# Kernel optimization log

Measured on AMD Instinct MI355X. Metric: run time of the kernel, lower is better.

## Reference

```python
import jax, jax.numpy as jnp
import numpy as np

N = 100_000
E = 1_600_000
IN, HID, HEADS, OUT = 128, 64, 4, 64
LAYER_DIMS = [(IN, HEADS, HID // HEADS), (HID, HEADS, HID // HEADS), (HID, 1, OUT)]
NEG_SLOPE = 0.2


def setup_inputs() -> dict:
    key = jax.random.key(0)
    ks = jax.random.split(key, 20)
    inp = {}
    inp["x"] = jax.random.normal(ks[0], (N, IN), dtype=jnp.float32)
    # edges with src != dst by construction (module removes self loops, then adds them)
    for i in range(3):
        src = jax.random.randint(ks[1 + 2 * i], (E,), 0, N, dtype=jnp.int32)
        off = jax.random.randint(ks[2 + 2 * i], (E,), 1, N, dtype=jnp.int32)
        dst = ((src + off) % N).astype(jnp.int32)
        inp[f"edge_index{i}"] = jnp.stack([src, dst])
    k = 7
    for i, (cin, h, c) in enumerate(LAYER_DIMS):
        ws = 1.0 / np.sqrt(cin)
        inp[f"Wl{i}"] = jax.random.normal(ks[k], (cin, h * c), dtype=jnp.float32) * ws; k += 1
        inp[f"bl{i}"] = jnp.zeros((h * c,), dtype=jnp.float32)
        inp[f"Wr{i}"] = jax.random.normal(ks[k], (cin, h * c), dtype=jnp.float32) * ws; k += 1
        inp[f"br{i}"] = jnp.zeros((h * c,), dtype=jnp.float32)
        inp[f"att{i}"] = jax.random.normal(ks[k], (h, c), dtype=jnp.float32) * (1.0 / np.sqrt(c)); k += 1
        inp[f"bias{i}"] = jnp.zeros((h * c,), dtype=jnp.float32)
    return inp


def _l1norm(x):
    return x / jnp.maximum(jnp.sum(jnp.abs(x), axis=1, keepdims=True), 1e-12)


def _gat2conv(x, ei, Wl, bl, Wr, br, att, bias, heads, out_c):
    n = x.shape[0]
    xl = (x @ Wl + bl).reshape(n, heads, out_c)  # source-side features (x_j)
    xr = (x @ Wr + br).reshape(n, heads, out_c)  # target-side features (x_i)
    src, dst = ei[0], ei[1]
    s = jax.nn.leaky_relu(xl[src] + xr[dst], NEG_SLOPE)      # [E', H, C]
    a = jnp.einsum('ehc,hc->eh', s, att)                      # [E', H]
    m = jax.ops.segment_max(a, dst, num_segments=n)           # segment softmax over edges per target
    e = jnp.exp(a - m[dst])
    den = jax.ops.segment_sum(e, dst, num_segments=n)
    alpha = e / (den[dst] + 1e-16)
    msg = (xl[src] * alpha[:, :, None]).reshape(-1, heads * out_c)
    return jax.ops.segment_sum(msg, dst, num_segments=n) + bias  # concat heads + bias


def _forward(x, eis, params):
    loop = jnp.arange(N, dtype=eis[0].dtype)
    self_loops = jnp.stack([loop, loop])
    num_layers = len(LAYER_DIMS)
    for i, ((cin, h, c), p) in enumerate(zip(LAYER_DIMS, params)):
        ei = jnp.concatenate([eis[i], self_loops], axis=1)  # add_self_loops
        new_x = _gat2conv(x, ei, *p, h, c)
        x = new_x
        if i != num_layers - 1:
            x = jax.nn.relu(new_x)
        x = _l1norm(x)  # F.normalize(x, p=1)
    x = x / jnp.maximum(jnp.linalg.norm(x, axis=1, keepdims=True), 1e-12)  # F.normalize (L2)
    return jax.nn.relu(x)


def reference(x, edge_index0, edge_index1, edge_index2,
              Wl0, bl0, Wr0, br0, att0, bias0,
              Wl1, bl1, Wr1, br1, att1, bias1,
              Wl2, bl2, Wr2, br2, att2, bias2):
    eis = (edge_index0, edge_index1, edge_index2)
    params = [(Wl0, bl0, Wr0, br0, att0, bias0),
              (Wl1, bl1, Wr1, br1, att1, bias1),
              (Wl2, bl2, Wr2, br2, att2, bias2)]
    return _forward(x, eis, params)
```

## Files before the change

### kernel.cpp

```cpp
#include <hip/hip_runtime.h>
#include <hip/hip_fp16.h>
#include <string.h>

#define NN 100000
#define EE 1600000
#define CAP 48
#define NBIN 196
#define BINSZ 512
#define BINCAP 10400
#define CHA 2048
#define NCA 782
#define GGX 391

typedef __fp16 h2v __attribute__((ext_vector_type(2)));
typedef __fp16 h4v __attribute__((ext_vector_type(4)));
typedef __fp16 half8 __attribute__((ext_vector_type(8)));
typedef float  f32x4 __attribute__((ext_vector_type(4)));

template<int CTRL>
__device__ __forceinline__ float dppadd(float x){
    int y = __builtin_amdgcn_update_dpp(0, __float_as_int(x), CTRL, 0xF, 0xF, true);
    return x + __int_as_float(y);
}
template<int H>
__device__ __forceinline__ float head_reduce16(float p){
    p = dppadd<0xB1>(p);
    p = dppadd<0x4E>(p);
    if constexpr (H == 1){
        p = dppadd<0x141>(p);
        p = dppadd<0x140>(p);
    }
    return p;
}
__device__ __forceinline__ float red16(float p){
    p = dppadd<0xB1>(p);
    p = dppadd<0x4E>(p);
    p = dppadd<0x141>(p);
    p = dppadd<0x140>(p);
    return p;
}


__global__ __launch_bounds__(256) void k_A(
    const int* __restrict__ e0, const int* __restrict__ e1, const int* __restrict__ e2,
    int* __restrict__ p0, int* __restrict__ p1, int* __restrict__ p2,
    int* __restrict__ tail)
{
    __shared__ int h4[4][NBIN];
    __shared__ int cur[NBIN];
    const int l = blockIdx.x / NCA, c = blockIdx.x % NCA;
    const int* ei = (l==0? e0 : l==1? e1 : e2);
    int* pr = (l==0? p0 : l==1? p1 : p2);
    const int base = c*CHA, n = min(CHA, EE-base);
    const int tid = threadIdx.x;
    const int wave = tid >> 6;
    for (int i=tid;i<4*NBIN;i+=256) ((int*)h4)[i]=0;
    __syncthreads();
    int dreg[CHA/256], sreg[CHA/256];
    #pragma unroll
    for (int j = 0; j < CHA/256; ++j){
        const int i = tid + j*256;
        if (i < n){ dreg[j] = ei[EE+base+i]; sreg[j] = ei[base+i]; }
        else { dreg[j] = -1; }
    }
    #pragma unroll
    for (int j = 0; j < CHA/256; ++j)
        if (dreg[j] >= 0) atomicAdd(&h4[wave][dreg[j]>>9],1);
    __syncthreads();
    if (tid < NBIN){
        const int t = h4[0][tid]+h4[1][tid]+h4[2][tid]+h4[3][tid];
        cur[tid] = t ? atomicAdd(&tail[l*NBIN+tid], t) : 0;
    }
    __syncthreads();
    #pragma unroll
    for (int j = 0; j < CHA/256; ++j){
        if (dreg[j] < 0) continue;
        const int d = dreg[j], s = sreg[j];
        const int bb = d>>9;
        const int r = atomicAdd(&cur[bb],1);
        if (r < BINCAP) pr[bb*BINCAP + r] = (s << 9) | (d & 511);
    }
}

__global__ __launch_bounds__(256) void k_B(
    const int* __restrict__ p0, const int* __restrict__ p1, const int* __restrict__ p2,
    const int* __restrict__ tail,
    int* __restrict__ c0, int* __restrict__ s0,
    int* __restrict__ c1, int* __restrict__ s1,
    int* __restrict__ c2, int* __restrict__ s2)
{
    __shared__ int cnt[BINSZ];
    __shared__ __align__(16) int sl[BINSZ*CAP];
    const int l = blockIdx.x / NBIN, b = blockIdx.x % NBIN;
    const int* pr = (l==0? p0 : l==1? p1 : p2) + (size_t)b*BINCAP;
    int* gc = (l==0? c0 : l==1? c1 : c2);
    int* gs = (l==0? s0 : l==1? s1 : s2);
    const int n0 = b*BINSZ;
    const int nn = min(BINSZ, NN - n0);
    const int tid = threadIdx.x;
    for (int i=tid;i<nn;i+=256){ cnt[i]=1; sl[i*CAP]= n0+i; }
    __syncthreads();
    const int ec = min(tail[l*NBIN+b], BINCAP);
    for (int i=tid;i<ec;i+=256){
        const int pv = pr[i];
        const int nd = pv & 511;
        const int p = atomicAdd(&cnt[nd],1);
        if (p < CAP) sl[nd*CAP+p] = pv >> 9;
    }
    __syncthreads();
    for (int i=tid;i<nn;i+=256) gc[n0+i] = cnt[i];
    const int t4 = nn*(CAP/4);
    int4* gs4 = (int4*)(gs + (size_t)n0*CAP);
    const int4* sl4 = (const int4*)sl;
    for (int i=tid;i<t4;i+=256) gs4[i] = sl4[i];
}


template<int CIN, typename TIN>
__global__ __launch_bounds__(256) void k_gemm(
    const TIN* __restrict__ x,
    const float* __restrict__ Wl, const float* __restrict__ bl,
    const float* __restrict__ Wr, const float* __restrict__ br,
    __half* __restrict__ xlh, float* __restrict__ xr)
{
    constexpr int KC = CIN / 32;
    const int tid = threadIdx.x;
    const int wave = tid >> 6, lane = tid & 63;
    const int m = lane & 15, g = lane >> 4;
    const int side = blockIdx.y;
    const float* __restrict__ W  = side ? Wr : Wl;
    const float* __restrict__ bb = side ? br : bl;

    half8 bf[4][KC];
    #pragma unroll
    for (int ct = 0; ct < 4; ++ct)
        #pragma unroll
        for (int kc = 0; kc < KC; ++kc)
            #pragma unroll
            for (int i = 0; i < 8; ++i)
                bf[ct][kc][i] = (__fp16)W[(kc*32 + g*8 + i)*64 + ct*16 + m];

    float bv[4];
    #pragma unroll
    for (int ct = 0; ct < 4; ++ct) bv[ct] = bb[ct*16 + m];

    const int stride = GGX * 64;
    for (int row0 = blockIdx.x*64 + wave*16; row0 < NN; row0 += stride){
        half8 a[KC];
        const TIN* xp = x + (size_t)(row0 + m) * CIN + g*8;
        #pragma unroll
        for (int kc = 0; kc < KC; ++kc){
            if constexpr (sizeof(TIN) == 4){
                const float4 u = *(const float4*)(xp + kc*32);
                const float4 v = *(const float4*)(xp + kc*32 + 4);
                a[kc][0]=(__fp16)u.x; a[kc][1]=(__fp16)u.y; a[kc][2]=(__fp16)u.z; a[kc][3]=(__fp16)u.w;
                a[kc][4]=(__fp16)v.x; a[kc][5]=(__fp16)v.y; a[kc][6]=(__fp16)v.z; a[kc][7]=(__fp16)v.w;
            } else {
                a[kc] = *(const half8*)(xp + kc*32);
            }
        }
        f32x4 acc0 = {0,0,0,0}, acc1 = {0,0,0,0}, acc2 = {0,0,0,0}, acc3 = {0,0,0,0};
        #pragma unroll
        for (int kc = 0; kc < KC; ++kc){
            acc0 = __builtin_amdgcn_mfma_f32_16x16x32_f16(a[kc], bf[0][kc], acc0, 0,0,0);
            acc1 = __builtin_amdgcn_mfma_f32_16x16x32_f16(a[kc], bf[1][kc], acc1, 0,0,0);
            acc2 = __builtin_amdgcn_mfma_f32_16x16x32_f16(a[kc], bf[2][kc], acc2, 0,0,0);
            acc3 = __builtin_amdgcn_mfma_f32_16x16x32_f16(a[kc], bf[3][kc], acc3, 0,0,0);
        }
        #pragma unroll
        for (int j = 0; j < 4; ++j){
            const size_t rb = (size_t)(row0 + 4*g + j)*64 + m;
            const float o0 = acc0[j] + bv[0];
            const float o1 = acc1[j] + bv[1];
            const float o2 = acc2[j] + bv[2];
            const float o3 = acc3[j] + bv[3];
            if (side){
                xr[rb]    = o0; xr[rb+16] = o1; xr[rb+32] = o2; xr[rb+48] = o3;
            } else {
                xlh[rb]    = __float2half_rn(o0);
                xlh[rb+16] = __float2half_rn(o1);
                xlh[rb+32] = __float2half_rn(o2);
                xlh[rb+48] = __float2half_rn(o3);
            }
        }
    }
}

template<int H, bool LAST>
__global__ __launch_bounds__(256) void k_fused(
    const int* __restrict__ cnt, const int* __restrict__ slots,
    const __half* __restrict__ xlh, const float* __restrict__ xr,
    const float* __restrict__ att, const float* __restrict__ bias,
    __half* __restrict__ o_h, float* __restrict__ o_f)
{
    const int lane = threadIdx.x & 63;
    const int sub = lane >> 4;
    const int c  = lane & 15;
    const int node = __builtin_amdgcn_readfirstlane(blockIdx.x * 4 + (threadIdx.x >> 6));
    if (node >= NN) return;
    constexpr float L2E = 1.44269504088896f;

    const float4 xr4 = *(const float4*)(xr + (size_t)node*64 + 4*c);
    const h2v xra = { (__fp16)xr4.x, (__fp16)xr4.y };
    const h2v xrb = { (__fp16)xr4.z, (__fp16)xr4.w };
    const float4 at4 = *(const float4*)(att + 4*c);
    const h2v ata = { (__fp16)(at4.x*L2E), (__fp16)(at4.y*L2E) };
    const h2v atb = { (__fp16)(at4.z*L2E), (__fp16)(at4.w*L2E) };
    const float4 b4 = *(const float4*)(bias + 4*c);
    const h2v k02 = { (__fp16)0.2f, (__fp16)0.2f };

    int deg = __builtin_amdgcn_readfirstlane(cnt[node]);
    deg = deg > CAP ? CAP : deg;
    const int dm1 = deg - 1;
    const int* __restrict__ sp = slots + (size_t)node * CAP;

    float den = 0.f, a0 = 0.f, a1 = 0.f, a2 = 0.f, a3 = 0.f;
    const int ngrp = (deg + 7) >> 3;

    for (int g = 0; g < ngrp; ++g){
        const int b0 = g*8;
        #pragma unroll
        for (int jj = 0; jj < 2; ++jj){
            const int eidx = b0 + 4*jj + sub;
            const int ec = eidx < dm1 ? eidx : dm1;
            const int id = sp[ec];
            const uint2 u = *(const uint2*)(xlh + (size_t)id*64 + 4*c);
            h2v xa, xb; memcpy(&xa, &u.x, 4); memcpy(&xb, &u.y, 4);
            h2v va = xa + xra, vb = xb + xrb;
            va = __builtin_elementwise_max(va, va * k02);
            vb = __builtin_elementwise_max(vb, vb * k02);
            float q = head_reduce16<H>(__builtin_amdgcn_fdot2(va, ata,
                        __builtin_amdgcn_fdot2(vb, atb, 0.f, false), false));
            q = (eidx <= dm1) ? q : -16384.f;
            const float e = __builtin_amdgcn_exp2f(q);
            a0 = fmaf(e, (float)xa[0], a0);
            a1 = fmaf(e, (float)xa[1], a1);
            a2 = fmaf(e, (float)xb[0], a2);
            a3 = fmaf(e, (float)xb[1], a3);
            den += e;
        }
    }
    a0 += __shfl_xor(a0,16); a0 += __shfl_xor(a0,32);
    a1 += __shfl_xor(a1,16); a1 += __shfl_xor(a1,32);
    a2 += __shfl_xor(a2,16); a2 += __shfl_xor(a2,32);
    a3 += __shfl_xor(a3,16); a3 += __shfl_xor(a3,32);
    den += __shfl_xor(den,16); den += __shfl_xor(den,32);

    const float rd = __builtin_amdgcn_rcpf(den);
    float o0 = fmaf(a0, rd, b4.x);
    float o1 = fmaf(a1, rd, b4.y);
    float o2 = fmaf(a2, rd, b4.z);
    float o3 = fmaf(a3, rd, b4.w);
    if (!LAST){ o0=fmaxf(o0,0.f); o1=fmaxf(o1,0.f); o2=fmaxf(o2,0.f); o3=fmaxf(o3,0.f); }
    const float ns = red16((fabsf(o0)+fabsf(o1)) + (fabsf(o2)+fabsf(o3)));
    const float rs = __builtin_amdgcn_rcpf(fmaxf(ns, 1e-12f));
    o0 *= rs; o1 *= rs; o2 *= rs; o3 *= rs;
    if (LAST){
        const float qq = red16((o0*o0+o1*o1) + (o2*o2+o3*o3));
        const float rq = __builtin_amdgcn_rsqf(fmaxf(qq, 1e-24f));
        o0=fmaxf(o0*rq,0.f); o1=fmaxf(o1*rq,0.f); o2=fmaxf(o2*rq,0.f); o3=fmaxf(o3*rq,0.f);
    }
    if (sub == 0){
        if constexpr (LAST){
            *(float4*)(o_f + (size_t)node*64 + 4*c) = make_float4(o0,o1,o2,o3);
        } else {
            h4v ov = { (__fp16)o0, (__fp16)o1, (__fp16)o2, (__fp16)o3 };
            *(h4v*)((__fp16*)o_h + (size_t)node*64 + 4*c) = ov;
        }
    }
}

__global__ __launch_bounds__(256) void k_init(int* __restrict__ cnt, int* __restrict__ slots)
{
    const int i = blockIdx.x * 256 + threadIdx.x;
    if (i < NN){ cnt[i] = 1; slots[(size_t)i * CAP] = i; }
}
__global__ __launch_bounds__(256) void k_build(
    const int* __restrict__ ei, int* __restrict__ cnt, int* __restrict__ slots)
{
    const int stride = gridDim.x * 256;
    for (int e = blockIdx.x * 256 + threadIdx.x; e < EE; e += stride){
        const int s = ei[e], d = ei[e + EE];
        const int pos = atomicAdd(&cnt[d], 1);
        if (pos < CAP) slots[(size_t)d * CAP + pos] = s;
    }
}

extern "C" void kernel_launch(void* const* d_in, const int* in_sizes, int n_in,
                              void* d_out, int out_size, void* d_ws, size_t ws_size,
                              hipStream_t stream)
{
    const float* x0 = (const float*)d_in[0];
    const int* ei[3] = {(const int*)d_in[1], (const int*)d_in[2], (const int*)d_in[3]};
    const float *Wl[3], *bl[3], *Wr[3], *br[3], *att[3], *bias[3];
    for (int i = 0; i < 3; ++i){
        Wl[i]   = (const float*)d_in[4 + 6*i];
        bl[i]   = (const float*)d_in[5 + 6*i];
        Wr[i]   = (const float*)d_in[6 + 6*i];
        br[i]   = (const float*)d_in[7 + 6*i];
        att[i]  = (const float*)d_in[8 + 6*i];
        bias[i] = (const float*)d_in[9 + 6*i];
    }
    float* out = (float*)d_out;

    const size_t NN64 = (size_t)NN * 64;
    __half* xlh = (__half*)d_ws;
    float*  xr  = (float*)((char*)d_ws + NN64*2);
    __half* xbh = (__half*)((char*)xr + NN64*4);
    int* base = (int*)((char*)xbh + NN64*2);

    const size_t fused_need = NN64*2 + NN64*4 + NN64*2 + (3*(size_t)NN*(CAP+1) + 3*NBIN)*4;

    dim3 blk(256);
    dim3 ggrid2(GGX, 2);
    const int ngrid = (NN + 3) / 4;
    const int igrid = (NN + 255) / 256;

    if (ws_size >= fused_need){
        int* c0 = base;                 int* s0 = c0 + NN;
        int* c1 = s0 + (size_t)NN*CAP;  int* s1 = c1 + NN;
        int* c2 = s1 + (size_t)NN*CAP;  int* s2 = c2 + NN;
        int* tail = s2 + (size_t)NN*CAP;
        int* p0 = (int*)out;
        int* p1 = (int*)d_ws;
        int* p2 = p1 + (size_t)NBIN*BINCAP;

        (void)hipMemsetAsync(tail, 0, 3*NBIN*sizeof(int), stream);
        k_A<<<3*NCA, blk, 0, stream>>>(ei[0], ei[1], ei[2], p0, p1, p2, tail);
        k_B<<<3*NBIN, blk, 0, stream>>>(p0, p1, p2, tail, c0, s0, c1, s1, c2, s2);

        k_gemm<128,float><<<ggrid2, blk, 0, stream>>>(x0, Wl[0], bl[0], Wr[0], br[0], xlh, xr);
        k_fused<4,false><<<ngrid, blk, 0, stream>>>(c0, s0, xlh, xr, att[0], bias[0], xbh, nullptr);
        k_gemm<64,__half><<<ggrid2, blk, 0, stream>>>(xbh, Wl[1], bl[1], Wr[1], br[1], xlh, xr);
        k_fused<4,false><<<ngrid, blk, 0, stream>>>(c1, s1, xlh, xr, att[1], bias[1], xbh, nullptr);
        k_gemm<64,__half><<<ggrid2, blk, 0, stream>>>(xbh, Wl[2], bl[2], Wr[2], br[2], xlh, xr);
        k_fused<1,true><<<ngrid, blk, 0, stream>>>(c2, s2, xlh, xr, att[2], bias[2], nullptr, out);
    } else {
        int* cnt = base;
        int* slots = cnt + NN;

        k_init<<<igrid, blk, 0, stream>>>(cnt, slots);
        k_gemm<128,float><<<ggrid2, blk, 0, stream>>>(x0, Wl[0], bl[0], Wr[0], br[0], xlh, xr);
        k_build<<<512, blk, 0, stream>>>(ei[0], cnt, slots);
        k_fused<4,false><<<ngrid, blk, 0, stream>>>(cnt, slots, xlh, xr, att[0], bias[0], xbh, nullptr);

        k_init<<<igrid, blk, 0, stream>>>(cnt, slots);
        k_gemm<64,__half><<<ggrid2, blk, 0, stream>>>(xbh, Wl[1], bl[1], Wr[1], br[1], xlh, xr);
        k_build<<<512, blk, 0, stream>>>(ei[1], cnt, slots);
        k_fused<4,false><<<ngrid, blk, 0, stream>>>(cnt, slots, xlh, xr, att[1], bias[1], xbh, nullptr);

        k_init<<<igrid, blk, 0, stream>>>(cnt, slots);
        k_gemm<64,__half><<<ggrid2, blk, 0, stream>>>(xbh, Wl[2], bl[2], Wr[2], br[2], xlh, xr);
        k_build<<<512, blk, 0, stream>>>(ei[2], cnt, slots);
        k_fused<1,true><<<ngrid, blk, 0, stream>>>(cnt, slots, xlh, xr, att[2], bias[2], nullptr, out);
    }
}
```

Before: 317.6 us.

## Co-schedule edge binning with layer-0 GEMM in one launch

Merges the edge-binning pass and the first-layer projection GEMM into a single kernel whose blocks are split by index, so both run concurrently. This removes a launch and lets the two independent stages share the GPU. The binning scratch buffers move into the output and xbh buffers so they no longer alias xlh, which the GEMM writes at the same time. Binning blocks now loop over chunks with a grid-stride. Both stages compete for memory bandwidth, which limits the overlap benefit.

```diff
diff --git a/kernel.cpp b/kernel.cpp
--- a/kernel.cpp
+++ b/kernel.cpp
@@ -10,6 +10,7 @@
 #define BINCAP 10400
 #define CHA 2048
 #define NCA 782
+#define NBA 1024
 #define GGX 391
 
 typedef __fp16 h2v __attribute__((ext_vector_type(2)));
@@ -41,16 +42,10 @@
 }
 
 
-__global__ __launch_bounds__(256) void k_A(
-    const int* __restrict__ e0, const int* __restrict__ e1, const int* __restrict__ e2,
-    int* __restrict__ p0, int* __restrict__ p1, int* __restrict__ p2,
-    int* __restrict__ tail)
-{
-    __shared__ int h4[4][NBIN];
-    __shared__ int cur[NBIN];
-    const int l = blockIdx.x / NCA, c = blockIdx.x % NCA;
-    const int* ei = (l==0? e0 : l==1? e1 : e2);
-    int* pr = (l==0? p0 : l==1? p1 : p2);
+__device__ __forceinline__ void dev_A_chunk(
+    int l, int c, const int* __restrict__ ei, int* __restrict__ pr,
+    int* __restrict__ tail, int (*h4)[NBIN], int* cur)
+{
     const int base = c*CHA, n = min(CHA, EE-base);
     const int tid = threadIdx.x;
     const int wave = tid >> 6;
@@ -80,45 +75,12 @@
         const int r = atomicAdd(&cur[bb],1);
         if (r < BINCAP) pr[bb*BINCAP + r] = (s << 9) | (d & 511);
     }
-}
-
-__global__ __launch_bounds__(256) void k_B(
-    const int* __restrict__ p0, const int* __restrict__ p1, const int* __restrict__ p2,
-    const int* __restrict__ tail,
-    int* __restrict__ c0, int* __restrict__ s0,
-    int* __restrict__ c1, int* __restrict__ s1,
-    int* __restrict__ c2, int* __restrict__ s2)
-{
-    __shared__ int cnt[BINSZ];
-    __shared__ __align__(16) int sl[BINSZ*CAP];
-    const int l = blockIdx.x / NBIN, b = blockIdx.x % NBIN;
-    const int* pr = (l==0? p0 : l==1? p1 : p2) + (size_t)b*BINCAP;
-    int* gc = (l==0? c0 : l==1? c1 : c2);
-    int* gs = (l==0? s0 : l==1? s1 : s2);
-    const int n0 = b*BINSZ;
-    const int nn = min(BINSZ, NN - n0);
-    const int tid = threadIdx.x;
-    for (int i=tid;i<nn;i+=256){ cnt[i]=1; sl[i*CAP]= n0+i; }
-    __syncthreads();
-    const int ec = min(tail[l*NBIN+b], BINCAP);
-    for (int i=tid;i<ec;i+=256){
-        const int pv = pr[i];
-        const int nd = pv & 511;
-        const int p = atomicAdd(&cnt[nd],1);
-        if (p < CAP) sl[nd*CAP+p] = pv >> 9;
-    }
-    __syncthreads();
-    for (int i=tid;i<nn;i+=256) gc[n0+i] = cnt[i];
-    const int t4 = nn*(CAP/4);
-    int4* gs4 = (int4*)(gs + (size_t)n0*CAP);
-    const int4* sl4 = (const int4*)sl;
-    for (int i=tid;i<t4;i+=256) gs4[i] = sl4[i];
-}
-
+    __syncthreads();
+}
 
 template<int CIN, typename TIN>
-__global__ __launch_bounds__(256) void k_gemm(
-    const TIN* __restrict__ x,
+__device__ __forceinline__ void dev_gemm(
+    int bx, int side, const TIN* __restrict__ x,
     const float* __restrict__ Wl, const float* __restrict__ bl,
     const float* __restrict__ Wr, const float* __restrict__ br,
     __half* __restrict__ xlh, float* __restrict__ xr)
@@ -127,7 +89,6 @@
     const int tid = threadIdx.x;
     const int wave = tid >> 6, lane = tid & 63;
     const int m = lane & 15, g = lane >> 4;
-    const int side = blockIdx.y;
     const float* __restrict__ W  = side ? Wr : Wl;
     const float* __restrict__ bb = side ? br : bl;
 
@@ -145,7 +106,7 @@
     for (int ct = 0; ct < 4; ++ct) bv[ct] = bb[ct*16 + m];
 
     const int stride = GGX * 64;
-    for (int row0 = blockIdx.x*64 + wave*16; row0 < NN; row0 += stride){
+    for (int row0 = bx*64 + wave*16; row0 < NN; row0 += stride){
         half8 a[KC];
         const TIN* xp = x + (size_t)(row0 + m) * CIN + g*8;
         #pragma unroll
@@ -184,6 +145,74 @@
             }
         }
     }
+}
+
+__global__ __launch_bounds__(256) void k_AG(
+    const int* __restrict__ e0, const int* __restrict__ e1, const int* __restrict__ e2,
+    int* __restrict__ p0, int* __restrict__ p1, int* __restrict__ p2,
+    int* __restrict__ tail,
+    const float* __restrict__ x,
+    const float* __restrict__ Wl, const float* __restrict__ bl,
+    const float* __restrict__ Wr, const float* __restrict__ br,
+    __half* __restrict__ xlh, float* __restrict__ xr)
+{
+    __shared__ int h4[4][NBIN];
+    __shared__ int cur[NBIN];
+    const int bid = blockIdx.x;
+    if (bid < NBA){
+        for (int ch = bid; ch < 3*NCA; ch += NBA){
+            const int l = ch / NCA, c = ch % NCA;
+            const int* ei = (l==0? e0 : l==1? e1 : e2);
+            int* pr = (l==0? p0 : l==1? p1 : p2);
+            dev_A_chunk(l, c, ei, pr, tail, h4, cur);
+        }
+    } else {
+        const int gb = bid - NBA;
+        dev_gemm<128,float>(gb % GGX, gb / GGX, x, Wl, bl, Wr, br, xlh, xr);
+    }
+}
+
+template<int CIN, typename TIN>
+__global__ __launch_bounds__(256) void k_gemm(
+    const TIN* __restrict__ x,
+    const float* __restrict__ Wl, const float* __restrict__ bl,
+    const float* __restrict__ Wr, const float* __restrict__ br,
+    __half* __restrict__ xlh, float* __restrict__ xr)
+{
+    dev_gemm<CIN,TIN>(blockIdx.x, blockIdx.y, x, Wl, bl, Wr, br, xlh, xr);
+}
+
+__global__ __launch_bounds__(256) void k_B(
+    const int* __restrict__ p0, const int* __restrict__ p1, const int* __restrict__ p2,
+    const int* __restrict__ tail,
+    int* __restrict__ c0, int* __restrict__ s0,
+    int* __restrict__ c1, int* __restrict__ s1,
+    int* __restrict__ c2, int* __restrict__ s2)
+{
+    __shared__ int cnt[BINSZ];
+    __shared__ __align__(16) int sl[BINSZ*CAP];
+    const int l = blockIdx.x / NBIN, b = blockIdx.x % NBIN;
+    const int* pr = (l==0? p0 : l==1? p1 : p2) + (size_t)b*BINCAP;
+    int* gc = (l==0? c0 : l==1? c1 : c2);
+    int* gs = (l==0? s0 : l==1? s1 : s2);
+    const int n0 = b*BINSZ;
+    const int nn = min(BINSZ, NN - n0);
+    const int tid = threadIdx.x;
+    for (int i=tid;i<nn;i+=256){ cnt[i]=1; sl[i*CAP]= n0+i; }
+    __syncthreads();
+    const int ec = min(tail[l*NBIN+b], BINCAP);
+    for (int i=tid;i<ec;i+=256){
+        const int pv = pr[i];
+        const int nd = pv & 511;
+        const int p = atomicAdd(&cnt[nd],1);
+        if (p < CAP) sl[nd*CAP+p] = pv >> 9;
+    }
+    __syncthreads();
+    for (int i=tid;i<nn;i+=256) gc[n0+i] = cnt[i];
+    const int t4 = nn*(CAP/4);
+    int4* gs4 = (int4*)(gs + (size_t)n0*CAP);
+    const int4* sl4 = (const int4*)sl;
+    for (int i=tid;i<t4;i+=256) gs4[i] = sl4[i];
 }
 
 template<int H, bool LAST>
@@ -322,14 +351,15 @@
         int* c2 = s1 + (size_t)NN*CAP;  int* s2 = c2 + NN;
         int* tail = s2 + (size_t)NN*CAP;
         int* p0 = (int*)out;
-        int* p1 = (int*)d_ws;
-        int* p2 = p1 + (size_t)NBIN*BINCAP;
+        int* p1 = p0 + (size_t)NBIN*BINCAP;
+        int* p2 = (int*)xbh;
 
         (void)hipMemsetAsync(tail, 0, 3*NBIN*sizeof(int), stream);
-        k_A<<<3*NCA, blk, 0, stream>>>(ei[0], ei[1], ei[2], p0, p1, p2, tail);
+        k_AG<<<NBA + 2*GGX, blk, 0, stream>>>(
+            ei[0], ei[1], ei[2], p0, p1, p2, tail,
+            x0, Wl[0], bl[0], Wr[0], br[0], xlh, xr);
         k_B<<<3*NBIN, blk, 0, stream>>>(p0, p1, p2, tail, c0, s0, c1, s1, c2, s2);
 
-        k_gemm<128,float><<<ggrid2, blk, 0, stream>>>(x0, Wl[0], bl[0], Wr[0], br[0], xlh, xr);
         k_fused<4,false><<<ngrid, blk, 0, stream>>>(c0, s0, xlh, xr, att[0], bias[0], xbh, nullptr);
         k_gemm<64,__half><<<ggrid2, blk, 0, stream>>>(xbh, Wl[1], bl[1], Wr[1], br[1], xlh, xr);
         k_fused<4,false><<<ngrid, blk, 0, stream>>>(c1, s1, xlh, xr, att[1], bias[1], xbh, nullptr);
```

New measurement: 311.5 us. No clear change (-1.9%).
